# Performance work log

Hardware: AMD Instinct MI355X
Metric: run time of the kernel (lower is better)

The kernel has to match this reference:

```python
import jax, jax.numpy as jnp
import numpy as np

BLOCK_SIZE = 64


def setup_inputs() -> dict:
    key = jax.random.key(0)
    kq, kk, kv, km = jax.random.split(key, 4)
    H, N, D = 16, 8192, 64
    nb = N // BLOCK_SIZE
    return {
        "q": jax.random.normal(kq, (H, N, D), dtype=jnp.float32),
        "k": jax.random.normal(kk, (H, N, D), dtype=jnp.float32),
        "v": jax.random.normal(kv, (H, N, D), dtype=jnp.float32),
        "block_mask": jax.random.randint(km, (nb, nb), 0, 2, dtype=jnp.int32),
    }


def reference(q, k, v, block_mask):
    """Block-sparse flash attention with online softmax.

    q, k, v: [H, N, D]; block_mask: [N//B, N//B] (1 = valid, 0 = masked).
    Scans over key blocks, processing all query rows at once; masked blocks
    contribute exactly zero (exp(-inf) = 0), matching the original's skip.
    """
    H, N, D = q.shape
    B = BLOCK_SIZE
    nb = N // B
    scale = D ** -0.5

    kb = k.reshape(H, nb, B, D).transpose(1, 0, 2, 3)  # [nb, H, B, D]
    vb = v.reshape(H, nb, B, D).transpose(1, 0, 2, 3)  # [nb, H, B, D]
    mask_cols = block_mask.T  # [nb_key, nb_query]: row j = validity of key block j per query block

    m0 = jnp.full((H, N, 1), -jnp.inf, dtype=q.dtype)
    l0 = jnp.zeros((H, N, 1), dtype=q.dtype)
    o0 = jnp.zeros((H, N, D), dtype=q.dtype)

    def step(carry, xs):
        m, l, o = carry
        k_j, v_j, mcol = xs  # k_j/v_j: [H, B, D]; mcol: [nb] over query blocks
        logits = jnp.einsum('hnd,hbd->hnb', q, k_j) * scale  # [H, N, B]
        valid = (jnp.repeat(mcol, B) > 0)[None, :, None]      # [1, N, 1]
        logits = jnp.where(valid, logits, -jnp.inf)
        m_new = jnp.maximum(m, logits.max(-1, keepdims=True))
        # guard: if everything so far is masked, m_new = -inf; use 0 to keep exps finite (=0)
        m_safe = jnp.where(jnp.isneginf(m_new), jnp.zeros_like(m_new), m_new)
        a_old = jnp.exp(m - m_safe)       # rescale of previous accumulators
        p = jnp.exp(logits - m_safe)      # masked entries -> 0
        l = a_old * l + p.sum(-1, keepdims=True)
        o = a_old * o + jnp.einsum('hnb,hbd->hnd', p, v_j)
        return (m_new, l, o), None

    (m, l, o), _ = jax.lax.scan(step, (m0, l0, o0), (kb, vb, mask_cols))
    return o / l
```

## Files before the change

### kernel.cpp

```cpp
#include <hip/hip_runtime.h>

#define Hh 16
#define Nn 8192
#define Dd 64
#define NB 128

typedef float  f32x4   __attribute__((ext_vector_type(4)));
typedef float  f32x16  __attribute__((ext_vector_type(16)));
typedef float  float4_ __attribute__((ext_vector_type(4)));
typedef short  bf16x8  __attribute__((ext_vector_type(8)));
typedef unsigned short ushort8  __attribute__((ext_vector_type(8)));
typedef unsigned short ushort4_ __attribute__((ext_vector_type(4)));

typedef const __attribute__((address_space(1))) unsigned int gu32;
typedef __attribute__((address_space(3))) unsigned int lu32;

#define QSCALE 0.1803368801111244f

__device__ __forceinline__ unsigned short f2bf(float f) {
    union { float f; unsigned u; } x; x.f = f;
    unsigned r = x.u + 0x7fffu + ((x.u >> 16) & 1u);
    return (unsigned short)(r >> 16);
}

__device__ __forceinline__ unsigned pack2bf(float lo, float hi) {
    return (unsigned)f2bf(lo) | ((unsigned)f2bf(hi) << 16);
}

__global__ void cvt_k(const float* __restrict__ k, unsigned short* __restrict__ ko) {
    int i = blockIdx.x * 256 + threadIdx.x;
    float4_ b = ((const float4_*)k)[i];
    ushort4_ ob;
#pragma unroll
    for (int j = 0; j < 4; ++j) ob[j] = f2bf(b[j]);
    ((ushort4_*)ko)[i] = ob;
}

__global__ void cvt_vt(const float* __restrict__ v, unsigned short* __restrict__ vt) {
    int jb = blockIdx.x, h = blockIdx.y, t = threadIdx.x;
    __shared__ float T[64][65];
    const float4_* src = (const float4_*)(v + ((long)h * Nn + jb * 64) * Dd);
#pragma unroll
    for (int it = 0; it < 4; ++it) {
        int r = (t >> 4) + it * 16;
        int c0 = (t & 15) * 4;
        float4_ x = src[r * 16 + (t & 15)];
#pragma unroll
        for (int i2 = 0; i2 < 4; ++i2) T[c0 + i2][r] = x[i2];
    }
    __syncthreads();
    int d = t >> 2, seg = (t & 3) * 16;
    ushort8 o0, o1;
#pragma unroll
    for (int i2 = 0; i2 < 8; ++i2) o0[i2] = f2bf(T[d][seg + i2]);
#pragma unroll
    for (int i2 = 0; i2 < 8; ++i2) o1[i2] = f2bf(T[d][seg + 8 + i2]);
    unsigned short* dst = vt + ((long)h * Dd + d) * Nn + jb * 64 + seg;
    *(ushort8*)dst = o0;
    *(ushort8*)(dst + 8) = o1;
}

__global__ __launch_bounds__(256, 4) void attn32(
        const unsigned short* __restrict__ k16,
        const unsigned short* __restrict__ vt16,
        const float* __restrict__ qf,
        const int* __restrict__ mask,
        float* __restrict__ out) {
    int bid = blockIdx.x;
    int h = (bid & 7) | ((bid >> 10) << 3);
    int qb = (bid >> 3) & 127;
    int tid = threadIdx.x;
    int wid = tid >> 6, l = tid & 63;
    int q5 = l & 31, hi = l >> 5;
    int qh = wid & 1;
    int kh = wid >> 1;
    int stage_kv = wid >> 1;
    int stage_half = wid & 1;

    __shared__ __align__(16) char smem[32768];

    const int* mrow = mask + qb * NB;
    unsigned long long b0 = __ballot(mrow[l] != 0);
    unsigned long long b1 = __ballot(mrow[64 + l] != 0);
    int count = __popcll(b0) + __popcll(b1);

    if (count == 0) {
        float4_ z = {0.f, 0.f, 0.f, 0.f};
        float4_* ob = (float4_*)(out + ((size_t)h * Nn + qb * 64) * Dd);
        for (int x = tid; x < 64 * 64 / 4; x += 256) ob[x] = z;
        return;
    }

    size_t qrow = (size_t)h * Nn + qb * 64 + qh * 32 + q5;
    bf16x8 qfrag[4];
#pragma unroll
    for (int ds_ = 0; ds_ < 4; ++ds_) {
        const float4_* qs = (const float4_*)(qf + qrow * Dd + ds_ * 16 + hi * 8);
        float4_ x = qs[0], y = qs[1];
        union { unsigned short s[8]; bf16x8 v; } u;
#pragma unroll
        for (int i2 = 0; i2 < 4; ++i2) {
            u.s[i2]     = f2bf(x[i2] * QSCALE);
            u.s[4 + i2] = f2bf(y[i2] * QSCALE);
        }
        qfrag[ds_] = u.v;
    }

    union { unsigned short s[8]; bf16x8 v; } ones;
#pragma unroll
    for (int i2 = 0; i2 < 8; ++i2) ones.s[i2] = 0x3F80;

    const unsigned short* sp[4];
    size_t jmul;
#pragma unroll
    for (int ff = 0; ff < 4; ++ff) {
        int f = stage_half * 4 + ff;
        if (stage_kv == 0)
            sp[ff] = k16 + (size_t)h * (Nn * Dd)
                   + (size_t)(q5 + 32 * (f >> 2)) * Dd + (f & 3) * 16 + hi * 8;
        else
            sp[ff] = vt16 + (size_t)h * (Nn * Dd)
                   + (size_t)(q5 + 32 * (f >> 2)) * Nn + (f & 3) * 16 + hi * 8;
    }
    jmul = (stage_kv == 0) ? (size_t)(64 * Dd) : (size_t)64;

    unsigned long long r0 = b0, r1 = b1;
    auto next_j = [&]() {
        int jj;
        if (r0) { jj = __ffsll(r0) - 1; r0 &= r0 - 1; }
        else    { jj = 63 + __ffsll(r1); r1 &= r1 - 1; }
        return jj;
    };

    auto issue = [&](int nbuf, int jj) {
        char* base = smem + (stage_kv ? 16384 : 0) + nbuf * 8192;
#pragma unroll
        for (int ff = 0; ff < 4; ++ff) {
            const unsigned short* g = sp[ff] + (size_t)jj * jmul;
            __builtin_amdgcn_global_load_lds((gu32*)g,
                (lu32*)(base + (stage_half * 4 + ff) * 1024), 16, 0, 0);
        }
    };

    issue(0, next_j());

    f32x16 o0 = {}, o1 = {}, ls = {};

    for (int i = 0; i < count; ++i) {
        int buf = i & 1;
        __syncthreads();
        if (i + 1 < count) issue(buf ^ 1, next_j());

        const char* kb = smem + buf * 8192 + kh * 4096 + l * 16;
        const char* vb = smem + 16384 + buf * 8192 + l * 16;

        f32x16 s = {};
#pragma unroll
        for (int ds_ = 0; ds_ < 4; ++ds_) {
            bf16x8 kf = *(const bf16x8*)(kb + ds_ * 1024);
            s = __builtin_amdgcn_mfma_f32_32x32x16_bf16(kf, qfrag[ds_], s, 0, 0, 0);
        }

#pragma unroll
        for (int e = 0; e < 16; ++e) s[e] = __builtin_amdgcn_exp2f(s[e]);

        unsigned w[8];
#pragma unroll
        for (int jj = 0; jj < 8; ++jj) w[jj] = pack2bf(s[2 * jj], s[2 * jj + 1]);
        auto swap32 = [&](unsigned& a, unsigned& b) {
            unsigned send = hi ? a : b;
            unsigned recv = (unsigned)__shfl_xor((int)send, 32);
            a = hi ? recv : a;
            b = hi ? b : recv;
        };
        swap32(w[0], w[2]); swap32(w[1], w[3]);
        swap32(w[4], w[6]); swap32(w[5], w[7]);

        union U { unsigned u[4]; bf16x8 v; };
        U pbs[2];
        pbs[0].u[0] = w[0]; pbs[0].u[1] = w[1]; pbs[0].u[2] = w[2]; pbs[0].u[3] = w[3];
        pbs[1].u[0] = w[4]; pbs[1].u[1] = w[5]; pbs[1].u[2] = w[6]; pbs[1].u[3] = w[7];

        int c0 = kh * 2;
#pragma unroll
        for (int sl = 0; sl < 2; ++sl) {
            bf16x8 vf0 = *(const bf16x8*)(vb + (c0 + sl) * 1024);
            o0 = __builtin_amdgcn_mfma_f32_32x32x16_bf16(vf0, pbs[sl].v, o0, 0, 0, 0);
        }
#pragma unroll
        for (int sl = 0; sl < 2; ++sl) {
            bf16x8 vf1 = *(const bf16x8*)(vb + 4096 + (c0 + sl) * 1024);
            o1 = __builtin_amdgcn_mfma_f32_32x32x16_bf16(vf1, pbs[sl].v, o1, 0, 0, 0);
        }
        ls = __builtin_amdgcn_mfma_f32_32x32x16_bf16(ones.v, pbs[0].v, ls, 0, 0, 0);
        ls = __builtin_amdgcn_mfma_f32_32x32x16_bf16(ones.v, pbs[1].v, ls, 0, 0, 0);
    }

    __syncthreads();
    float* comb = (float*)smem;
    if (kh == 1) {
        float* dst = comb + (qh * 64 + l) * 33;
#pragma unroll
        for (int e = 0; e < 16; ++e) { dst[e] = o0[e]; dst[16 + e] = o1[e]; }
        dst[32] = ls[0];
    }
    __syncthreads();
    if (kh == 0) {
        const float* src = comb + (qh * 64 + l) * 33;
#pragma unroll
        for (int e = 0; e < 16; ++e) { o0[e] += src[e]; o1[e] += src[16 + e]; }
        float inv = 1.0f / (ls[0] + src[32]);

        float* obase = out + qrow * Dd;
#pragma unroll
        for (int s4 = 0; s4 < 4; ++s4) {
            float4_ t0, t1;
#pragma unroll
            for (int e = 0; e < 4; ++e) { t0[e] = o0[4 * s4 + e] * inv; t1[e] = o1[4 * s4 + e] * inv; }
            *(float4_*)(obase + 8 * s4 + 4 * hi)      = t0;
            *(float4_*)(obase + 32 + 8 * s4 + 4 * hi) = t1;
        }
    }
}

__global__ void attn_main(const float* __restrict__ qf, const float* __restrict__ kf,
                          const float* __restrict__ vf, const int* __restrict__ mask,
                          float* __restrict__ out) {
    int id = blockIdx.x;
    int h = id & 15, qb = id >> 4;
    int tid = threadIdx.x;
    int lane = tid & 63, wid = tid >> 6;
    int l15 = lane & 15, l4 = lane >> 4;

    __shared__ unsigned short Kl[2][64 * 64];
    __shared__ unsigned short Vl[2][64 * 64];
    __shared__ unsigned short Pl[4][16 * 64];

    const int* mrow = mask + qb * NB;
    unsigned long long b0 = __ballot(mrow[lane] != 0);
    unsigned long long b1 = __ballot(mrow[64 + lane] != 0);
    int count = __popcll(b0) + __popcll(b1);

    float* op = out + ((long)h * Nn + qb * 64 + wid * 16) * Dd;

    if (count == 0) {
#pragma unroll
        for (int r = 0; r < 4; ++r)
#pragma unroll
            for (int dn = 0; dn < 4; ++dn)
                op[(l4 * 4 + r) * Dd + dn * 16 + l15] = 0.f;
        return;
    }

    long qrow = (long)h * Nn + qb * 64 + wid * 16 + l15;
    bf16x8 qfrag[2];
#pragma unroll
    for (int dc = 0; dc < 2; ++dc) {
        const float4_* qs = (const float4_*)qf + qrow * 16 + dc * 8 + l4 * 2;
        float4_ x = qs[0], y = qs[1];
        union { unsigned short s[8]; bf16x8 v; } u;
#pragma unroll
        for (int i2 = 0; i2 < 4; ++i2) {
            u.s[i2] = f2bf(x[i2] * 0.125f);
            u.s[4 + i2] = f2bf(y[i2] * 0.125f);
        }
        qfrag[dc] = u.v;
    }

    int sgq = tid & 7;
    int srow = tid >> 3;
    float4_ kf4[2][2]; float4_ vf4[4];
    int vk = tid & 63, vd0 = (tid >> 6) * 16;

    auto load_kv = [&](int j) {
        const float4_* ks = (const float4_*)kf + ((long)h * Nn + j * 64) * 16;
#pragma unroll
        for (int it = 0; it < 2; ++it) {
            kf4[it][0] = ks[(srow + it * 32) * 16 + sgq * 2];
            kf4[it][1] = ks[(srow + it * 32) * 16 + sgq * 2 + 1];
        }
        const float4_* vs = (const float4_*)vf + ((long)h * Nn + j * 64) * 16;
#pragma unroll
        for (int c = 0; c < 4; ++c) vf4[c] = vs[vk * 16 + (vd0 >> 2) + c];
    };

    auto write_kv = [&](int buf) {
#pragma unroll
        for (int it = 0; it < 2; ++it) {
            int r = srow + it * 32;
            union { unsigned short s[8]; ushort8 v; } u;
#pragma unroll
            for (int i2 = 0; i2 < 4; ++i2) {
                u.s[i2] = f2bf(kf4[it][0][i2]);
                u.s[4 + i2] = f2bf(kf4[it][1][i2]);
            }
            *(ushort8*)((char*)&Kl[buf][0] + r * 128 + (((sgq ^ r) & 7) << 4)) = u.v;
        }
#pragma unroll
        for (int i2 = 0; i2 < 16; ++i2) {
            int d = vd0 + i2;
            *((unsigned short*)((char*)&Vl[buf][0] + d * 128 +
                ((((vk >> 3) ^ d) & 7) << 4) + ((vk & 7) << 1))) = f2bf(vf4[i2 >> 2][i2 & 3]);
        }
    };

    f32x4 o_acc[4] = {};
    float m_r[4], l_r[4];
#pragma unroll
    for (int r = 0; r < 4; ++r) { m_r[r] = -INFINITY; l_r[r] = 0.f; }

    unsigned long long r0 = b0, r1 = b1;
    auto next_j = [&]() {
        int jj;
        if (r0) { jj = __ffsll(r0) - 1; r0 &= r0 - 1; }
        else    { jj = 63 + __ffsll(r1); r1 &= r1 - 1; }
        return jj;
    };

    load_kv(next_j());

    for (int i = 0; i < count; ++i) {
        int buf = i & 1;
        write_kv(buf);
        __syncthreads();
        if (i + 1 < count) load_kv(next_j());

        f32x4 s[4] = {};
#pragma unroll
        for (int dc = 0; dc < 2; ++dc) {
#pragma unroll
            for (int kn = 0; kn < 4; ++kn) {
                int krow = kn * 16 + l15;
                bf16x8 kfr = *(const bf16x8*)((const char*)&Kl[buf][0] +
                               krow * 128 + ((((l4 + dc * 4) ^ krow) & 7) << 4));
                s[kn] = __builtin_amdgcn_mfma_f32_16x16x32_bf16(qfrag[dc], kfr, s[kn], 0, 0, 0);
            }
        }

#pragma unroll
        for (int r = 0; r < 4; ++r) {
            float mx = fmaxf(fmaxf(s[0][r], s[1][r]), fmaxf(s[2][r], s[3][r]));
#pragma unroll
            for (int off = 1; off < 16; off <<= 1) mx = fmaxf(mx, __shfl_xor(mx, off));
            float mn = fmaxf(m_r[r], mx);
            float a = __expf(m_r[r] - mn);
            m_r[r] = mn;
            float psum = 0.f;
#pragma unroll
            for (int kn = 0; kn < 4; ++kn) { float p = __expf(s[kn][r] - mn); s[kn][r] = p; psum += p; }
#pragma unroll
            for (int off = 1; off < 16; off <<= 1) psum += __shfl_xor(psum, off);
            l_r[r] = l_r[r] * a + psum;
            o_acc[0][r] *= a; o_acc[1][r] *= a; o_acc[2][r] *= a; o_acc[3][r] *= a;
        }

#pragma unroll
        for (int kn = 0; kn < 4; ++kn) {
#pragma unroll
            for (int r = 0; r < 4; ++r) {
                int prow = l4 * 4 + r;
                int pc = kn * 16 + l15;
                *((unsigned short*)((char*)&Pl[wid][0] + prow * 128 +
                    ((((pc >> 3) ^ prow) & 7) << 4) + ((pc & 7) << 1))) = f2bf(s[kn][r]);
            }
        }

        bf16x8 pa[2];
#pragma unroll
        for (int kc = 0; kc < 2; ++kc)
            pa[kc] = *(const bf16x8*)((const char*)&Pl[wid][0] +
                      l15 * 128 + ((((l4 + kc * 4) ^ l15) & 7) << 4));
#pragma unroll
        for (int dn = 0; dn < 4; ++dn) {
            int vrow = dn * 16 + l15;
#pragma unroll
            for (int kc = 0; kc < 2; ++kc) {
                bf16x8 vbf = *(const bf16x8*)((const char*)&Vl[buf][0] +
                             vrow * 128 + ((((l4 + kc * 4) ^ vrow) & 7) << 4));
                o_acc[dn] = __builtin_amdgcn_mfma_f32_16x16x32_bf16(pa[kc], vbf, o_acc[dn], 0, 0, 0);
            }
        }
    }

#pragma unroll
    for (int r = 0; r < 4; ++r) {
        float inv = 1.0f / l_r[r];
#pragma unroll
        for (int dn = 0; dn < 4; ++dn)
            op[(l4 * 4 + r) * Dd + dn * 16 + l15] = o_acc[dn][r] * inv;
    }
}

extern "C" void kernel_launch(void* const* d_in, const int* in_sizes, int n_in,
                              void* d_out, int out_size, void* d_ws, size_t ws_size,
                              hipStream_t stream) {
    const float* q = (const float*)d_in[0];
    const float* k = (const float*)d_in[1];
    const float* v = (const float*)d_in[2];
    const int* mask = (const int*)d_in[3];
    float* out = (float*)d_out;

    size_t elems = (size_t)Hh * Nn * Dd;
    size_t need = 2 * elems * sizeof(unsigned short);
    if (ws_size >= need) {
        unsigned short* k16 = (unsigned short*)d_ws;
        unsigned short* vt16 = k16 + elems;
        cvt_k<<<dim3((unsigned)(elems / 1024)), 256, 0, stream>>>(k, k16);
        cvt_vt<<<dim3(NB, Hh), 256, 0, stream>>>(v, vt16);
        attn32<<<dim3(Hh * NB), 256, 0, stream>>>(k16, vt16, q, mask, out);
    } else {
        attn_main<<<dim3(Hh * NB), 256, 0, stream>>>(q, k, v, mask, out);
    }
}
```

Measured before the change: 341.4 us.

## Replace 4-wave LDS-staged block with single-wave register-prefetch attention kernel

The 256-thread attention block, which staged K/V tiles through LDS with global_load_lds and barriers and split keys across waves, becomes a 64-thread single-wave kernel. Each wave owns 32 query rows and processes the full 64-key block, loading K and V fragments straight from global memory into registers and prefetching the next block's data during compute. Row sums are now computed with VALU adds and a cross-half shuffle instead of MFMAs against a ones vector, and the LDS cross-wave combine is removed. The aim is to drop barrier and LDS traffic and raise occupancy via twice as many blocks. The cost is heavier register pressure and no reuse of K/V between waves through shared memory, so global and L2 traffic rises.

```diff
diff --git a/kernel.cpp b/kernel.cpp
--- a/kernel.cpp
+++ b/kernel.cpp
@@ -12,9 +12,6 @@
 typedef unsigned short ushort8  __attribute__((ext_vector_type(8)));
 typedef unsigned short ushort4_ __attribute__((ext_vector_type(4)));
 
-typedef const __attribute__((address_space(1))) unsigned int gu32;
-typedef __attribute__((address_space(3))) unsigned int lu32;
-
 #define QSCALE 0.1803368801111244f
 
 __device__ __forceinline__ unsigned short f2bf(float f) {
@@ -60,38 +57,37 @@
     *(ushort8*)(dst + 8) = o1;
 }
 
-__global__ __launch_bounds__(256, 4) void attn32(
+__global__ __launch_bounds__(64, 4) void attn_w(
         const unsigned short* __restrict__ k16,
         const unsigned short* __restrict__ vt16,
         const float* __restrict__ qf,
         const int* __restrict__ mask,
         float* __restrict__ out) {
     int bid = blockIdx.x;
-    int h = (bid & 7) | ((bid >> 10) << 3);
-    int qb = (bid >> 3) & 127;
-    int tid = threadIdx.x;
-    int wid = tid >> 6, l = tid & 63;
+    int xcd = bid & 7;
+    int i5 = bid >> 3;
+    int hhi = i5 >> 8;
+    int qb = (i5 >> 1) & 127;
+    int qhalf = i5 & 1;
+    int h = xcd | (hhi << 3);
+    int l = threadIdx.x;
     int q5 = l & 31, hi = l >> 5;
-    int qh = wid & 1;
-    int kh = wid >> 1;
-    int stage_kv = wid >> 1;
-    int stage_half = wid & 1;
-
-    __shared__ __align__(16) char smem[32768];
 
     const int* mrow = mask + qb * NB;
     unsigned long long b0 = __ballot(mrow[l] != 0);
     unsigned long long b1 = __ballot(mrow[64 + l] != 0);
     int count = __popcll(b0) + __popcll(b1);
 
+    size_t qrow = (size_t)h * Nn + qb * 64 + qhalf * 32 + q5;
+
     if (count == 0) {
         float4_ z = {0.f, 0.f, 0.f, 0.f};
-        float4_* ob = (float4_*)(out + ((size_t)h * Nn + qb * 64) * Dd);
-        for (int x = tid; x < 64 * 64 / 4; x += 256) ob[x] = z;
+        float4_* ob = (float4_*)(out + ((size_t)h * Nn + qb * 64 + qhalf * 32) * Dd);
+#pragma unroll
+        for (int c = 0; c < 8; ++c) ob[(l >> 1) * 16 + (l & 1) * 8 + c] = z;
         return;
     }
 
-    size_t qrow = (size_t)h * Nn + qb * 64 + qh * 32 + q5;
     bf16x8 qfrag[4];
 #pragma unroll
     for (int ds_ = 0; ds_ < 4; ++ds_) {
@@ -106,23 +102,14 @@
         qfrag[ds_] = u.v;
     }
 
-    union { unsigned short s[8]; bf16x8 v; } ones;
-#pragma unroll
-    for (int i2 = 0; i2 < 8; ++i2) ones.s[i2] = 0x3F80;
-
-    const unsigned short* sp[4];
-    size_t jmul;
-#pragma unroll
-    for (int ff = 0; ff < 4; ++ff) {
-        int f = stage_half * 4 + ff;
-        if (stage_kv == 0)
-            sp[ff] = k16 + (size_t)h * (Nn * Dd)
-                   + (size_t)(q5 + 32 * (f >> 2)) * Dd + (f & 3) * 16 + hi * 8;
-        else
-            sp[ff] = vt16 + (size_t)h * (Nn * Dd)
-                   + (size_t)(q5 + 32 * (f >> 2)) * Nn + (f & 3) * 16 + hi * 8;
-    }
-    jmul = (stage_kv == 0) ? (size_t)(64 * Dd) : (size_t)64;
+    const unsigned short* kbase = k16 + (size_t)h * (Nn * Dd);
+    const unsigned short* vbase = vt16 + (size_t)h * (Nn * Dd);
+    int koff[8], voff[8];
+#pragma unroll
+    for (int f = 0; f < 8; ++f) {
+        koff[f] = (q5 + 32 * (f >> 2)) * Dd + (f & 3) * 16 + hi * 8;
+        voff[f] = (q5 + 32 * (f >> 2)) * Nn + (f & 3) * 16 + hi * 8;
+    }
 
     unsigned long long r0 = b0, r1 = b1;
     auto next_j = [&]() {
@@ -132,94 +119,118 @@
         return jj;
     };
 
-    auto issue = [&](int nbuf, int jj) {
-        char* base = smem + (stage_kv ? 16384 : 0) + nbuf * 8192;
-#pragma unroll
-        for (int ff = 0; ff < 4; ++ff) {
-            const unsigned short* g = sp[ff] + (size_t)jj * jmul;
-            __builtin_amdgcn_global_load_lds((gu32*)g,
-                (lu32*)(base + (stage_half * 4 + ff) * 1024), 16, 0, 0);
-        }
+    bf16x8 kst[8], vst[8];
+    int jn = next_j();
+    {
+        const unsigned short* kj = kbase + (size_t)jn * (64 * Dd);
+        const unsigned short* vj = vbase + (size_t)jn * 64;
+#pragma unroll
+        for (int f = 0; f < 8; ++f) kst[f] = *(const bf16x8*)(kj + koff[f]);
+#pragma unroll
+        for (int f = 0; f < 8; ++f) vst[f] = *(const bf16x8*)(vj + voff[f]);
+    }
+
+    f32x16 o0 = {}, o1 = {};
+    float l_run = 0.f;
+
+    union U { unsigned u[4]; bf16x8 v; };
+    U pbs[4];
+
+    auto swap32 = [&](unsigned& a, unsigned& b) {
+        unsigned send = hi ? a : b;
+        unsigned recv = (unsigned)__shfl_xor((int)send, 32);
+        a = hi ? recv : a;
+        b = hi ? b : recv;
     };
 
-    issue(0, next_j());
-
-    f32x16 o0 = {}, o1 = {}, ls = {};
-
-    for (int i = 0; i < count; ++i) {
-        int buf = i & 1;
-        __syncthreads();
-        if (i + 1 < count) issue(buf ^ 1, next_j());
-
-        const char* kb = smem + buf * 8192 + kh * 4096 + l * 16;
-        const char* vb = smem + 16384 + buf * 8192 + l * 16;
+    for (int it = 0; it < count; ++it) {
+        bool have_next = (it + 1 < count);
 
         f32x16 s = {};
 #pragma unroll
-        for (int ds_ = 0; ds_ < 4; ++ds_) {
-            bf16x8 kf = *(const bf16x8*)(kb + ds_ * 1024);
-            s = __builtin_amdgcn_mfma_f32_32x32x16_bf16(kf, qfrag[ds_], s, 0, 0, 0);
-        }
-
+        for (int ds_ = 0; ds_ < 4; ++ds_)
+            s = __builtin_amdgcn_mfma_f32_32x32x16_bf16(kst[ds_], qfrag[ds_], s, 0, 0, 0);
 #pragma unroll
         for (int e = 0; e < 16; ++e) s[e] = __builtin_amdgcn_exp2f(s[e]);
-
-        unsigned w[8];
-#pragma unroll
-        for (int jj = 0; jj < 8; ++jj) w[jj] = pack2bf(s[2 * jj], s[2 * jj + 1]);
-        auto swap32 = [&](unsigned& a, unsigned& b) {
-            unsigned send = hi ? a : b;
-            unsigned recv = (unsigned)__shfl_xor((int)send, 32);
-            a = hi ? recv : a;
-            b = hi ? b : recv;
-        };
-        swap32(w[0], w[2]); swap32(w[1], w[3]);
-        swap32(w[4], w[6]); swap32(w[5], w[7]);
-
-        union U { unsigned u[4]; bf16x8 v; };
-        U pbs[2];
-        pbs[0].u[0] = w[0]; pbs[0].u[1] = w[1]; pbs[0].u[2] = w[2]; pbs[0].u[3] = w[3];
-        pbs[1].u[0] = w[4]; pbs[1].u[1] = w[5]; pbs[1].u[2] = w[6]; pbs[1].u[3] = w[7];
-
-        int c0 = kh * 2;
-#pragma unroll
-        for (int sl = 0; sl < 2; ++sl) {
-            bf16x8 vf0 = *(const bf16x8*)(vb + (c0 + sl) * 1024);
-            o0 = __builtin_amdgcn_mfma_f32_32x32x16_bf16(vf0, pbs[sl].v, o0, 0, 0, 0);
-        }
-#pragma unroll
-        for (int sl = 0; sl < 2; ++sl) {
-            bf16x8 vf1 = *(const bf16x8*)(vb + 4096 + (c0 + sl) * 1024);
-            o1 = __builtin_amdgcn_mfma_f32_32x32x16_bf16(vf1, pbs[sl].v, o1, 0, 0, 0);
-        }
-        ls = __builtin_amdgcn_mfma_f32_32x32x16_bf16(ones.v, pbs[0].v, ls, 0, 0, 0);
-        ls = __builtin_amdgcn_mfma_f32_32x32x16_bf16(ones.v, pbs[1].v, ls, 0, 0, 0);
-    }
-
-    __syncthreads();
-    float* comb = (float*)smem;
-    if (kh == 1) {
-        float* dst = comb + (qh * 64 + l) * 33;
-#pragma unroll
-        for (int e = 0; e < 16; ++e) { dst[e] = o0[e]; dst[16 + e] = o1[e]; }
-        dst[32] = ls[0];
-    }
-    __syncthreads();
-    if (kh == 0) {
-        const float* src = comb + (qh * 64 + l) * 33;
-#pragma unroll
-        for (int e = 0; e < 16; ++e) { o0[e] += src[e]; o1[e] += src[16 + e]; }
-        float inv = 1.0f / (ls[0] + src[32]);
-
-        float* obase = out + qrow * Dd;
-#pragma unroll
-        for (int s4 = 0; s4 < 4; ++s4) {
-            float4_ t0, t1;
-#pragma unroll
-            for (int e = 0; e < 4; ++e) { t0[e] = o0[4 * s4 + e] * inv; t1[e] = o1[4 * s4 + e] * inv; }
-            *(float4_*)(obase + 8 * s4 + 4 * hi)      = t0;
-            *(float4_*)(obase + 32 + 8 * s4 + 4 * hi) = t1;
-        }
+        float lpA;
+        {
+            float t8[8];
+#pragma unroll
+            for (int e = 0; e < 8; ++e) t8[e] = s[e] + s[e + 8];
+#pragma unroll
+            for (int e = 0; e < 4; ++e) t8[e] += t8[e + 4];
+            lpA = (t8[0] + t8[1]) + (t8[2] + t8[3]);
+        }
+        {
+            unsigned w[8];
+#pragma unroll
+            for (int jj = 0; jj < 8; ++jj) w[jj] = pack2bf(s[2 * jj], s[2 * jj + 1]);
+            swap32(w[0], w[2]); swap32(w[1], w[3]);
+            swap32(w[4], w[6]); swap32(w[5], w[7]);
+            pbs[0].u[0] = w[0]; pbs[0].u[1] = w[1]; pbs[0].u[2] = w[2]; pbs[0].u[3] = w[3];
+            pbs[1].u[0] = w[4]; pbs[1].u[1] = w[5]; pbs[1].u[2] = w[6]; pbs[1].u[3] = w[7];
+        }
+
+        f32x16 s2 = {};
+#pragma unroll
+        for (int ds_ = 0; ds_ < 4; ++ds_)
+            s2 = __builtin_amdgcn_mfma_f32_32x32x16_bf16(kst[4 + ds_], qfrag[ds_], s2, 0, 0, 0);
+
+        if (have_next) {
+            jn = next_j();
+            const unsigned short* kj = kbase + (size_t)jn * (64 * Dd);
+#pragma unroll
+            for (int f = 0; f < 8; ++f) kst[f] = *(const bf16x8*)(kj + koff[f]);
+        }
+
+#pragma unroll
+        for (int e = 0; e < 16; ++e) s2[e] = __builtin_amdgcn_exp2f(s2[e]);
+        float lpB;
+        {
+            float t8[8];
+#pragma unroll
+            for (int e = 0; e < 8; ++e) t8[e] = s2[e] + s2[e + 8];
+#pragma unroll
+            for (int e = 0; e < 4; ++e) t8[e] += t8[e + 4];
+            lpB = (t8[0] + t8[1]) + (t8[2] + t8[3]);
+        }
+        {
+            unsigned w[8];
+#pragma unroll
+            for (int jj = 0; jj < 8; ++jj) w[jj] = pack2bf(s2[2 * jj], s2[2 * jj + 1]);
+            swap32(w[0], w[2]); swap32(w[1], w[3]);
+            swap32(w[4], w[6]); swap32(w[5], w[7]);
+            pbs[2].u[0] = w[0]; pbs[2].u[1] = w[1]; pbs[2].u[2] = w[2]; pbs[2].u[3] = w[3];
+            pbs[3].u[0] = w[4]; pbs[3].u[1] = w[5]; pbs[3].u[2] = w[6]; pbs[3].u[3] = w[7];
+        }
+
+        float ps = lpA + lpB;
+        ps += __shfl_xor(ps, 32);
+        l_run += ps;
+
+#pragma unroll
+        for (int c = 0; c < 4; ++c)
+            o0 = __builtin_amdgcn_mfma_f32_32x32x16_bf16(vst[c], pbs[c].v, o0, 0, 0, 0);
+#pragma unroll
+        for (int c = 0; c < 4; ++c)
+            o1 = __builtin_amdgcn_mfma_f32_32x32x16_bf16(vst[4 + c], pbs[c].v, o1, 0, 0, 0);
+
+        if (have_next) {
+            const unsigned short* vj = vbase + (size_t)jn * 64;
+#pragma unroll
+            for (int f = 0; f < 8; ++f) vst[f] = *(const bf16x8*)(vj + voff[f]);
+        }
+    }
+
+    float inv = 1.0f / l_run;
+    float* obase = out + qrow * Dd;
+#pragma unroll
+    for (int s4 = 0; s4 < 4; ++s4) {
+        float4_ t0, t1;
+#pragma unroll
+        for (int e = 0; e < 4; ++e) { t0[e] = o0[4 * s4 + e] * inv; t1[e] = o1[4 * s4 + e] * inv; }
+        *(float4_*)(obase + 8 * s4 + 4 * hi)      = t0;
+        *(float4_*)(obase + 32 + 8 * s4 + 4 * hi) = t1;
     }
 }
 
@@ -407,7 +418,7 @@
         unsigned short* vt16 = k16 + elems;
         cvt_k<<<dim3((unsigned)(elems / 1024)), 256, 0, stream>>>(k, k16);
         cvt_vt<<<dim3(NB, Hh), 256, 0, stream>>>(v, vt16);
-        attn32<<<dim3(Hh * NB), 256, 0, stream>>>(k16, vt16, q, mask, out);
+        attn_w<<<dim3(Hh * NB * 2), 64, 0, stream>>>(k16, vt16, q, mask, out);
     } else {
         attn_main<<<dim3(Hh * NB), 256, 0, stream>>>(q, k, v, mask, out);
     }
```

Measured after the change: 1.069 ms. 213% more time.
